# Kernel optimization log

Hardware: AMD Instinct MI355X
Metric: run time of the kernel (lower is better)

The kernel has to match this reference:

```python
import jax, jax.numpy as jnp
import numpy as np

B, M, NT, V, D, H, E, S = 4, 12, 12, 10000, 64, 3, 512, 32


def setup_inputs() -> dict:
    key = jax.random.key(0)
    ks = jax.random.split(key, 16)
    def rn(k, shape, scale=0.05):
        return jax.random.normal(k, shape, dtype=jnp.float32) * scale
    return {
        "tendency": jax.random.normal(ks[0], (B, M, V), dtype=jnp.float32),
        "periodicity": jax.random.normal(ks[1], (B, NT, V), dtype=jnp.float32),
        "edges": jax.random.randint(ks[2], (H, E, S), 0, V),
        "w1": rn(ks[3], (1, D)), "b1": rn(ks[4], (D,)),
        "w2": rn(ks[5], (D, D)), "b2": rn(ks[6], (D,)),
        "attn_w": rn(ks[7], (D, D)), "attn_a": rn(ks[8], (2 * D, 1)),
        "w_ih": rn(ks[9], (4 * D, D)), "w_hh": rn(ks[10], (4 * D, D)),
        "b_ih": rn(ks[11], (4 * D,)), "b_hh": rn(ks[12], (4 * D,)),
        "w_out": rn(ks[13], (2 * D, 1)), "b_out": rn(ks[14], (1,)),
    }


def _hypersage(X, edges, w, b):
    # X: (N, V, F); edges: (E, S) node indices. All edges have size S <= Q,
    # so torch's random subsampling is the identity.
    n, v, f = X.shape
    e, s = edges.shape
    gathered = X[:, edges, :]                      # (N, E, S, F)
    agg = gathered.mean(axis=2)                    # (N, E, F)
    flat = edges.reshape(-1)                       # (E*S,)
    contrib = jnp.broadcast_to(agg[:, :, None, :], (n, e, s, f)).reshape(n, e * s, f)
    X_out = jnp.zeros((n, v, f), X.dtype).at[:, flat, :].add(contrib)
    deg = jnp.zeros((v,), X.dtype).at[flat].add(1.0)
    deg = jnp.maximum(deg, 1.0)
    X_out = X_out / deg[None, :, None]
    return X_out @ w + b                           # Linear fc


def _attention(Xs, attn_w, attn_a):
    # Xs: (H, N, V, D)
    ref = Xs.mean(axis=0)                          # (N, V, D)
    wx = Xs @ attn_w                               # (H, N, V, D)
    wr = ref @ attn_w                              # (N, V, D)
    z = jnp.concatenate([wx, jnp.broadcast_to(wr[None], wx.shape)], axis=-1) @ attn_a
    z = jax.nn.leaky_relu(z, negative_slope=0.2)   # (H, N, V, 1)
    alpha = jax.nn.softmax(z, axis=0)
    return (alpha * Xs).sum(axis=0)                # (N, V, D)


def _lstm_final(x, w_ih, w_hh, b_ih, b_hh):
    # x: (BV, T, D) -> final hidden state (BV, D). PyTorch gate order i,f,g,o.
    bv, t, d = x.shape
    xg = x @ w_ih.T + (b_ih + b_hh)                # precompute input gates (BV, T, 4D)
    def step(carry, xg_t):
        h, c = carry
        g = xg_t + h @ w_hh.T
        i, f, gg, o = jnp.split(g, 4, axis=-1)
        c = jax.nn.sigmoid(f) * c + jax.nn.sigmoid(i) * jnp.tanh(gg)
        h = jax.nn.sigmoid(o) * jnp.tanh(c)
        return (h, c), None
    h0 = jnp.zeros((bv, d), x.dtype)
    (h, _), _ = jax.lax.scan(step, (h0, h0), jnp.swapaxes(xg, 0, 1))
    return h


def _branch(seq, edges, w1, b1, w2, b2, attn_w, attn_a, w_ih, w_hh, b_ih, b_hh):
    b, t, v = seq.shape
    X = seq.reshape(b * t, v, 1)                   # fold time into batch (same DAMHG per step)
    def per_hg(e):
        return _hypersage(_hypersage(X, e, w1, b1), e, w2, b2)
    xs = jax.vmap(per_hg)(edges)                   # (H, B*T, V, D)
    fused = _attention(xs, attn_w, attn_a)         # (B*T, V, D)
    d = fused.shape[-1]
    seq_v = fused.reshape(b, t, v, d).transpose(0, 2, 1, 3).reshape(b * v, t, d)
    h = _lstm_final(seq_v, w_ih, w_hh, b_ih, b_hh)
    return h.reshape(b, v, d)


def reference(tendency, periodicity, edges, w1, b1, w2, b2, attn_w, attn_a, w_ih, w_hh, b_ih, b_hh, w_out, b_out):
    h_t = _branch(tendency, edges, w1, b1, w2, b2, attn_w, attn_a, w_ih, w_hh, b_ih, b_hh)
    h_p = _branch(periodicity, edges, w1, b1, w2, b2, attn_w, attn_a, w_ih, w_hh, b_ih, b_hh)
    fusion = jnp.concatenate([h_t, h_p], axis=-1)  # (B, V, 2D)
    out = fusion @ w_out + b_out                   # (B, V, 1)
    return out[..., 0]
```

## Files before the change

### kernel.cpp

```cpp
#include <hip/hip_runtime.h>

#define NV 10000
#define NB 4
#define NTT 12
#define NSEQ 48
#define NH 3
#define NE 512
#define NS 32
#define ND 64

#define S_U   0
#define S_C1  64
#define S_V1  128
#define S_V2  192
#define S_SC  256
#define S_GU  272
#define S_GC  528
#define S_G0  784
#define F_INV 1040
#define F_M   (F_INV + NH*NV)
#define F_PQ  (F_M + NH*NV)
#define F_HT  (F_PQ + 4*NV*NSEQ)
#define I_CNT (F_HT + 2*NB*NV)
#define I_CUR (I_CNT + NH*NV)
#define I_OFF (I_CUR + NH*NV)
#define I_SLOT (I_OFF + NH*NV)
#define F_DYN (I_SLOT + NH*NE*NS)
#define XT_SZ  (NV*NSEQ)
#define AGG_SZ (NH*NE*NSEQ)
#define YZ_SZ  (NH*NV*NSEQ)

typedef __attribute__((ext_vector_type(8))) _Float16 f16x8;
typedef __attribute__((ext_vector_type(4))) float f32x4;

__device__ __forceinline__ float sigf(float x) {
  return __builtin_amdgcn_rcpf(1.0f + __expf(-x));
}
__device__ __forceinline__ float tanh_fast(float x) {
  return 1.0f - 2.0f * __builtin_amdgcn_rcpf(1.0f + __expf(2.0f * x));
}
__device__ __forceinline__ unsigned short f2h(float x) {
  union { _Float16 h; unsigned short u; } c;
  c.h = (_Float16)x;
  return c.u;
}
__device__ __forceinline__ f16x8 ldsH(const unsigned short* p) {
  union { uint4 u; f16x8 v; } x;
  x.u = *(const uint4*)p;
  return x.v;
}

__global__ void k_prep(const float* __restrict__ w1, const float* __restrict__ b1,
                       const float* __restrict__ w2, const float* __restrict__ b2,
                       const float* __restrict__ attn_w, const float* __restrict__ attn_a,
                       const float* __restrict__ w_ih, const float* __restrict__ b_ih,
                       const float* __restrict__ b_hh, float* __restrict__ ws) {
  __shared__ float u_s[64], c1_s[64];
  const int tid = threadIdx.x;
  if (tid < 64) {
    float v1 = 0.f, v2 = 0.f, u = 0.f, c1 = 0.f;
    for (int d = 0; d < 64; ++d) {
      const float aw = attn_w[tid * 64 + d];
      v1 += aw * attn_a[d];
      v2 += aw * attn_a[64 + d];
      const float w2v = w2[d * 64 + tid];
      u  += w1[d] * w2v;
      c1 += b1[d] * w2v;
    }
    ws[S_U + tid] = u;  ws[S_C1 + tid] = c1;
    ws[S_V1 + tid] = v1; ws[S_V2 + tid] = v2;
    u_s[tid] = u; c1_s[tid] = c1;
  }
  __syncthreads();
  if (tid == 0) {
    float al = 0.f, be = 0.f, ga = 0.f, de = 0.f, ep = 0.f;
    for (int d = 0; d < 64; ++d) {
      const float v1 = ws[S_V1 + d], v2 = ws[S_V2 + d];
      al += u_s[d] * v1;  be += c1_s[d] * v1;
      ga += u_s[d] * v2;  de += c1_s[d] * v2;
      ep += b2[d] * (v1 + v2);
    }
    ws[S_SC + 0] = al; ws[S_SC + 1] = be; ws[S_SC + 2] = ga;
    ws[S_SC + 3] = de; ws[S_SC + 4] = ep;
  }
  {
    const int j = tid;
    float gu = 0.f, gc = 0.f, g0 = 0.f;
    for (int d = 0; d < 64; ++d) {
      const float w = w_ih[j * 64 + d];
      gu += w * u_s[d]; gc += w * c1_s[d]; g0 += w * b2[d];
    }
    ws[S_GU + j] = gu; ws[S_GC + j] = gc;
    ws[S_G0 + j] = g0 + b_ih[j] + b_hh[j];
  }
}

__global__ void k_zero(int* __restrict__ p, int n) {
  const int g = blockIdx.x * 256 + threadIdx.x;
  if (g < n) p[g] = 0;
}

__global__ void k_count(const int* __restrict__ edges, int* __restrict__ counts) {
  const int g = blockIdx.x * 256 + threadIdx.x;
  if (g >= NH * NE * NS) return;
  const int h = g >> 14;
  atomicAdd(&counts[h * NV + edges[g]], 1);
}

__global__ void k_scan(const int* __restrict__ counts, int* __restrict__ offs,
                       float* __restrict__ invdeg, float* __restrict__ mvec) {
  const int h = blockIdx.x;
  const int tid = threadIdx.x;
  const int base = h * NV;
  const int CH = 10;
  int local[10];
  int run = 0;
  for (int i = 0; i < CH; ++i) {
    const int v = tid * CH + i;
    const int c = (v < NV) ? counts[base + v] : 0;
    local[i] = run; run += c;
  }
  __shared__ int sd[1024];
  sd[tid] = run;
  __syncthreads();
  int acc = run;
  for (int off = 1; off < 1024; off <<= 1) {
    const int t = (tid >= off) ? sd[tid - off] : 0;
    __syncthreads();
    acc += t; sd[tid] = acc;
    __syncthreads();
  }
  const int excl = acc - run;
  for (int i = 0; i < CH; ++i) {
    const int v = tid * CH + i;
    if (v < NV) {
      offs[base + v] = excl + local[i];
      const int c = counts[base + v];
      invdeg[base + v] = 1.0f / (float)((c > 0) ? c : 1);
      mvec[base + v] = (c > 0) ? 1.0f : 0.0f;
    }
  }
}

__global__ void k_fill(const int* __restrict__ edges, const int* __restrict__ offs,
                       int* __restrict__ cursor, int* __restrict__ slot_edge) {
  const int g = blockIdx.x * 256 + threadIdx.x;
  if (g >= NH * NE * NS) return;
  const int h = g >> 14;
  const int e = (g >> 5) & (NE - 1);
  const int v = edges[g];
  const int pos = atomicAdd(&cursor[h * NV + v], 1);
  slot_edge[h * NE * NS + offs[h * NV + v] + pos] = e;
}

__global__ void k_trans2(const float* __restrict__ s0, const float* __restrict__ s1,
                         float* __restrict__ xT, int xtS) {
  __shared__ float tile[128][49];
  const float* seq = blockIdx.y ? s1 : s0;
  float* o = xT + (size_t)blockIdx.y * xtS;
  const int v0 = blockIdx.x * 128;
  const int tid = threadIdx.x;
  for (int i = tid; i < 128 * NSEQ; i += 256) {
    const int n = i / 128, vl = i % 128;
    const int v = v0 + vl;
    tile[vl][n] = (v < NV) ? seq[n * NV + v] : 0.0f;
  }
  __syncthreads();
  for (int i = tid; i < 128 * NSEQ; i += 256) {
    const int vl = i / NSEQ, n = i % NSEQ;
    const int v = v0 + vl;
    if (v < NV) o[v * NSEQ + n] = tile[vl][n];
  }
}

__global__ void k_eagg1(const int* __restrict__ edges, const float* __restrict__ xT,
                        int xtS, float* __restrict__ agg, int aggS) {
  const int g = blockIdx.x * 256 + threadIdx.x;
  if (g >= NH * NE * 12) return;
  const float* x = xT + (size_t)blockIdx.y * xtS;
  float* a = agg + (size_t)blockIdx.y * aggS;
  const int n0 = (g % 12) * 4;
  const int e = (g / 12) % NE;
  const int h = g / (12 * NE);
  const int* ep = edges + (h * NE + e) * NS;
  float4 acc = make_float4(0.f, 0.f, 0.f, 0.f);
  for (int s = 0; s < NS; ++s) {
    const float4 t = *(const float4*)&x[ep[s] * NSEQ + n0];
    acc.x += t.x; acc.y += t.y; acc.z += t.z; acc.w += t.w;
  }
  acc.x *= (1.0f / NS); acc.y *= (1.0f / NS); acc.z *= (1.0f / NS); acc.w *= (1.0f / NS);
  *(float4*)&a[(h * NE + e) * NSEQ + n0] = acc;
}

__global__ void k_eagg2(const int* __restrict__ edges, const float* __restrict__ ysum,
                        int yS, const float* __restrict__ invdeg,
                        float* __restrict__ agg, int aggS) {
  const int g = blockIdx.x * 256 + threadIdx.x;
  if (g >= NH * NE * 12) return;
  const float* y = ysum + (size_t)blockIdx.y * yS;
  float* a = agg + (size_t)blockIdx.y * aggS;
  const int n0 = (g % 12) * 4;
  const int e = (g / 12) % NE;
  const int h = g / (12 * NE);
  const int* ep = edges + (h * NE + e) * NS;
  float4 acc = make_float4(0.f, 0.f, 0.f, 0.f);
  for (int s = 0; s < NS; ++s) {
    const int v = ep[s];
    const float iv = invdeg[h * NV + v];
    const float4 t = *(const float4*)&y[(h * NV + v) * NSEQ + n0];
    acc.x += t.x * iv; acc.y += t.y * iv; acc.z += t.z * iv; acc.w += t.w * iv;
  }
  acc.x *= (1.0f / NS); acc.y *= (1.0f / NS); acc.z *= (1.0f / NS); acc.w *= (1.0f / NS);
  *(float4*)&a[(h * NE + e) * NSEQ + n0] = acc;
}

__global__ void k_vg(const int* __restrict__ counts, const int* __restrict__ offs,
                     const int* __restrict__ slot_edge, const float* __restrict__ agg,
                     int aggS, float* __restrict__ outv, int outS) {
  const int g = blockIdx.x * 256 + threadIdx.x;
  if (g >= NH * NV * 12) return;
  const float* a = agg + (size_t)blockIdx.y * aggS;
  float* o = outv + (size_t)blockIdx.y * outS;
  const int n0 = (g % 12) * 4;
  const int v = (g / 12) % NV;
  const int h = g / (12 * NV);
  const int beg = offs[h * NV + v];
  const int cnt = counts[h * NV + v];
  const int* se = slot_edge + h * NE * NS;
  float4 acc = make_float4(0.f, 0.f, 0.f, 0.f);
  for (int i = 0; i < cnt; ++i) {
    const int e = se[beg + i];
    const float4 t = *(const float4*)&a[(h * NE + e) * NSEQ + n0];
    acc.x += t.x; acc.y += t.y; acc.z += t.z; acc.w += t.w;
  }
  *(float4*)&o[(h * NV + v) * NSEQ + n0] = acc;
}

__global__ void k_attn(const float* __restrict__ zsum, int zS,
                       const float* __restrict__ invdeg, const float* __restrict__ mvec,
                       const float* __restrict__ ws, float* __restrict__ pq, int br0) {
  const int g = blockIdx.x * 256 + threadIdx.x;
  if (g >= NV * 12) return;
  const int bi = blockIdx.y;
  const float* z = zsum + (size_t)bi * zS;
  float* pbuf = pq + (size_t)(bi + br0) * 2 * NV * NSEQ;
  float* qbuf = pbuf + NV * NSEQ;
  const int n0 = (g % 12) * 4;
  const int v = g / 12;
  const float al = ws[S_SC + 0], be = ws[S_SC + 1], ga = ws[S_SC + 2],
              de = ws[S_SC + 3], ep = ws[S_SC + 4];
  union { float4 v4; float f[4]; } zh[3], pv, qv;
  float mh[3];
  #pragma unroll
  for (int h = 0; h < NH; ++h) {
    const float iv = invdeg[h * NV + v];
    float4 t = *(const float4*)&z[(h * NV + v) * NSEQ + n0];
    t.x *= iv; t.y *= iv; t.z *= iv; t.w *= iv;
    zh[h].v4 = t;
    mh[h] = mvec[h * NV + v];
  }
  const float mb = (mh[0] + mh[1] + mh[2]) * (1.f / 3.f);
  #pragma unroll
  for (int j = 0; j < 4; ++j) {
    const float z0 = zh[0].f[j], z1 = zh[1].f[j], z2 = zh[2].f[j];
    const float zb = (z0 + z1 + z2) * (1.f / 3.f);
    float sc[3];
    const float zt[3] = {z0, z1, z2};
    #pragma unroll
    for (int h = 0; h < NH; ++h) {
      const float s = al * zt[h] + be * mh[h] + ga * zb + de * mb + ep;
      sc[h] = (s > 0.f) ? s : 0.2f * s;
    }
    const float mx = fmaxf(sc[0], fmaxf(sc[1], sc[2]));
    const float e0 = __expf(sc[0] - mx), e1 = __expf(sc[1] - mx), e2 = __expf(sc[2] - mx);
    const float inv = 1.0f / (e0 + e1 + e2);
    pv.f[j] = (e0 * z0 + e1 * z1 + e2 * z2) * inv;
    qv.f[j] = (e0 * mh[0] + e1 * mh[1] + e2 * mh[2]) * inv;
  }
  *(float4*)&pbuf[v * NSEQ + n0] = pv.v4;
  *(float4*)&qbuf[v * NSEQ + n0] = qv.v4;
}

#define RS2 72
__launch_bounds__(256, 2)
__global__ void k_lstm2(const float* __restrict__ w_hh, const float* __restrict__ ws,
                        const float* __restrict__ pbase, const float* __restrict__ w_out,
                        float* __restrict__ part) {
  __shared__ __align__(16) unsigned short smem[16384];
  __shared__ float ps_sh[NTT][64], qs_sh[NTT][64];
  const int tid = threadIdx.x;
  const int w = tid >> 6, lane = tid & 63, q = lane >> 4, l15 = lane & 15;
  const int b = blockIdx.y, br = blockIdx.z;
  const int v0 = blockIdx.x * 64;
  const int d = w * 16 + l15;

  for (int i = tid; i < 4096; i += 256) {
    const float4 w4 = ((const float4*)w_hh)[i];
    const int j = i >> 4, k = (i & 15) * 4;
    uint2 pk;
    pk.x = (unsigned int)f2h(w4.x) | ((unsigned int)f2h(w4.y) << 16);
    pk.y = (unsigned int)f2h(w4.z) | ((unsigned int)f2h(w4.w) << 16);
    *(uint2*)&smem[j * 64 + k] = pk;
  }
  const float* pp = pbase + (size_t)br * 2 * NV * NSEQ;
  const float* qq = pp + NV * NSEQ;
  for (int i = tid; i < 384; i += 256) {
    const int arr = (i >= 192) ? 1 : 0;
    const int ii = i - arr * 192;
    const int s = ii / 3, f4 = ii % 3;
    const int v = v0 + s;
    const float* src = arr ? qq : pp;
    float4 val = make_float4(0.f, 0.f, 0.f, 0.f);
    if (v < NV) val = *(const float4*)&src[v * NSEQ + b * NTT + f4 * 4];
    float (*dst)[64] = arr ? qs_sh : ps_sh;
    dst[f4 * 4 + 0][s] = val.x; dst[f4 * 4 + 1][s] = val.y;
    dst[f4 * 4 + 2][s] = val.z; dst[f4 * 4 + 3][s] = val.w;
  }
  __syncthreads();

  f16x8 Bf[4][2];
  #pragma unroll
  for (int g = 0; g < 4; ++g)
    #pragma unroll
    for (int kh = 0; kh < 2; ++kh)
      Bf[g][kh] = ldsH(&smem[(g * 64 + d) * 64 + kh * 32 + q * 8]);

  union HU { uint4 u; f16x8 v; };
  HU bex[4];
  #pragma unroll
  for (int g = 0; g < 4; ++g) {
    const float gu = ws[S_GU + g * 64 + d];
    const float gc = ws[S_GC + g * 64 + d];
    const float g0 = ws[S_G0 + g * 64 + d];
    bex[g].u.x = (q == 0) ? ((unsigned int)f2h(gu) | ((unsigned int)f2h(gc) << 16)) : 0u;
    bex[g].u.y = (q == 0) ? (unsigned int)f2h(g0) : 0u;
    bex[g].u.z = 0u; bex[g].u.w = 0u;
  }
  const float WO = w_out[br * 64 + d];
  __syncthreads();

  f32x4 acc[4][4];
  f32x4 cst[4];
  float pr[4][4];
  #pragma unroll
  for (int mi = 0; mi < 4; ++mi) cst[mi] = (f32x4){0.f, 0.f, 0.f, 0.f};
  const f32x4 z4 = (f32x4){0.f, 0.f, 0.f, 0.f};

  #pragma unroll 1
  for (int t = 0; t < NTT; ++t) {
    #pragma unroll
    for (int mi = 0; mi < 4; ++mi) {
      HU ae;
      const float pv = ps_sh[t][mi * 16 + l15];
      const float qv = qs_sh[t][mi * 16 + l15];
      ae.u.x = (q == 0) ? ((unsigned int)f2h(pv) | ((unsigned int)f2h(qv) << 16)) : 0u;
      ae.u.y = (q == 0) ? 0x3C00u : 0u;
      ae.u.z = 0u; ae.u.w = 0u;
      #pragma unroll
      for (int g = 0; g < 4; ++g)
        acc[mi][g] = __builtin_amdgcn_mfma_f32_16x16x32_f16(ae.v, bex[g].v, z4, 0, 0, 0);
    }
    if (t > 0) {
      const unsigned short* hr = smem + ((t - 1) & 1) * (64 * RS2);
      #pragma unroll
      for (int kh = 0; kh < 2; ++kh)
        #pragma unroll
        for (int mi = 0; mi < 4; ++mi) {
          const int row = mi * 16 + l15;
          const f16x8 Ah = ldsH(&hr[row * RS2 + kh * 32 + q * 8]);
          #pragma unroll
          for (int g = 0; g < 4; ++g)
            acc[mi][g] = __builtin_amdgcn_mfma_f32_16x16x32_f16(Ah, Bf[g][kh], acc[mi][g], 0, 0, 0);
        }
    }
    unsigned short* hw = smem + (t & 1) * (64 * RS2);
    const bool last = (t == NTT - 1);
    #pragma unroll
    for (int mi = 0; mi < 4; ++mi)
      #pragma unroll
      for (int r = 0; r < 4; ++r) {
        const float ig = sigf(acc[mi][0][r]);
        const float fg = sigf(acc[mi][1][r]);
        const float gg = tanh_fast(acc[mi][2][r]);
        const float og = sigf(acc[mi][3][r]);
        const float cn = fmaf(fg, cst[mi][r], ig * gg);
        cst[mi][r] = cn;
        const float h = og * tanh_fast(cn);
        const int s = mi * 16 + q * 4 + r;
        if (!last) {
          hw[s * RS2 + d] = f2h(h);
        } else {
          pr[mi][r] = h * WO;
        }
      }
    __syncthreads();
  }
  float* fbuf = (float*)smem;
  #pragma unroll
  for (int mi = 0; mi < 4; ++mi)
    #pragma unroll
    for (int r = 0; r < 4; ++r) {
      float v = pr[mi][r];
      v += __shfl_xor(v, 1);
      v += __shfl_xor(v, 2);
      v += __shfl_xor(v, 4);
      v += __shfl_xor(v, 8);
      if (l15 == 0) fbuf[w * 64 + mi * 16 + q * 4 + r] = v;
    }
  __syncthreads();
  if (tid < 64) {
    const int v = v0 + tid;
    if (v < NV)
      part[(br * NB + b) * NV + v] =
          fbuf[tid] + fbuf[64 + tid] + fbuf[128 + tid] + fbuf[192 + tid];
  }
}

__global__ void k_comb(const float* __restrict__ part, const float* __restrict__ b_out,
                       float* __restrict__ out) {
  const int g = blockIdx.x * 256 + threadIdx.x;
  if (g >= NB * NV / 4) return;
  const float4 a = ((const float4*)part)[g];
  const float4 c = ((const float4*)part)[NB * NV / 4 + g];
  const float bo = b_out[0];
  float4 o;
  o.x = a.x + c.x + bo; o.y = a.y + c.y + bo;
  o.z = a.z + c.z + bo; o.w = a.w + c.w + bo;
  ((float4*)out)[g] = o;
}

extern "C" void kernel_launch(void* const* d_in, const int* in_sizes, int n_in,
                              void* d_out, int out_size, void* d_ws, size_t ws_size,
                              hipStream_t stream) {
  const float* tend   = (const float*)d_in[0];
  const float* peri   = (const float*)d_in[1];
  const int*   edges  = (const int*)d_in[2];
  const float* w1     = (const float*)d_in[3];
  const float* b1     = (const float*)d_in[4];
  const float* w2     = (const float*)d_in[5];
  const float* b2     = (const float*)d_in[6];
  const float* attn_w = (const float*)d_in[7];
  const float* attn_a = (const float*)d_in[8];
  const float* w_ih   = (const float*)d_in[9];
  const float* w_hh   = (const float*)d_in[10];
  const float* b_ih   = (const float*)d_in[11];
  const float* b_hh   = (const float*)d_in[12];
  const float* w_out  = (const float*)d_in[13];
  const float* b_out  = (const float*)d_in[14];
  float* out = (float*)d_out;
  float* ws  = (float*)d_ws;
  int*   iws = (int*)d_ws;
  int* cnt = iws + I_CNT;
  int* cur = iws + I_CUR;
  int* off = iws + I_OFF;
  int* sed = iws + I_SLOT;

  const size_t need2 = ((size_t)F_DYN + 2 * (XT_SZ + AGG_SZ + YZ_SZ)) * 4;
  const bool batched = ws_size >= need2;
  const int nb = batched ? 2 : 1;
  float* XT  = ws + F_DYN;
  float* AGG = XT + (size_t)nb * XT_SZ;
  float* YZ  = AGG + (size_t)nb * AGG_SZ;

  k_prep<<<1, 256, 0, stream>>>(w1, b1, w2, b2, attn_w, attn_a, w_ih, b_ih, b_hh, ws);
  k_zero<<<(2 * NH * NV + 255) / 256, 256, 0, stream>>>(cnt, 2 * NH * NV);
  k_count<<<(NH * NE * NS) / 256, 256, 0, stream>>>(edges, cnt);
  k_scan<<<NH, 1024, 0, stream>>>(cnt, off, ws + F_INV, ws + F_M);
  k_fill<<<(NH * NE * NS) / 256, 256, 0, stream>>>(edges, off, cur, sed);

  const int g_eagg = (NH * NE * 12 + 255) / 256;
  const int g_vg   = (NH * NV * 12 + 255) / 256;
  const int g_attn = (NV * 12 + 255) / 256;
  if (batched) {
    k_trans2<<<dim3((NV + 127) / 128, 2), 256, 0, stream>>>(tend, peri, XT, XT_SZ);
    k_eagg1<<<dim3(g_eagg, 2), 256, 0, stream>>>(edges, XT, XT_SZ, AGG, AGG_SZ);
    k_vg<<<dim3(g_vg, 2), 256, 0, stream>>>(cnt, off, sed, AGG, AGG_SZ, YZ, YZ_SZ);
    k_eagg2<<<dim3(g_eagg, 2), 256, 0, stream>>>(edges, YZ, YZ_SZ, ws + F_INV, AGG, AGG_SZ);
    k_vg<<<dim3(g_vg, 2), 256, 0, stream>>>(cnt, off, sed, AGG, AGG_SZ, YZ, YZ_SZ);
    k_attn<<<dim3(g_attn, 2), 256, 0, stream>>>(YZ, YZ_SZ, ws + F_INV, ws + F_M, ws, ws + F_PQ, 0);
  } else {
    for (int br = 0; br < 2; ++br) {
      const float* seq = br ? peri : tend;
      k_trans2<<<dim3((NV + 127) / 128, 1), 256, 0, stream>>>(seq, seq, XT, 0);
      k_eagg1<<<dim3(g_eagg, 1), 256, 0, stream>>>(edges, XT, 0, AGG, 0);
      k_vg<<<dim3(g_vg, 1), 256, 0, stream>>>(cnt, off, sed, AGG, 0, YZ, 0);
      k_eagg2<<<dim3(g_eagg, 1), 256, 0, stream>>>(edges, YZ, 0, ws + F_INV, AGG, 0);
      k_vg<<<dim3(g_vg, 1), 256, 0, stream>>>(cnt, off, sed, AGG, 0, YZ, 0);
      k_attn<<<dim3(g_attn, 1), 256, 0, stream>>>(YZ, 0, ws + F_INV, ws + F_M, ws, ws + F_PQ, br);
    }
  }
  dim3 lgrid((NV + 63) / 64, NB, 2);
  k_lstm2<<<lgrid, 256, 0, stream>>>(w_hh, ws, ws + F_PQ, w_out, ws + F_HT);
  k_comb<<<(NB * NV / 4 + 255) / 256, 256, 0, stream>>>(ws + F_HT, b_out, out);
}
```

Before: 262.0 us.

## Shrink LSTM LDS, load recurrent weights directly, interleave gates per row block

```diff
diff --git a/kernel.cpp b/kernel.cpp
--- a/kernel.cpp
+++ b/kernel.cpp
@@ -36,9 +36,6 @@
 __device__ __forceinline__ float sigf(float x) {
   return __builtin_amdgcn_rcpf(1.0f + __expf(-x));
 }
-__device__ __forceinline__ float tanh_fast(float x) {
-  return 1.0f - 2.0f * __builtin_amdgcn_rcpf(1.0f + __expf(2.0f * x));
-}
 __device__ __forceinline__ unsigned short f2h(float x) {
   union { _Float16 h; unsigned short u; } c;
   c.h = (_Float16)x;
@@ -282,11 +279,11 @@
 }
 
 #define RS2 72
-__launch_bounds__(256, 2)
+__launch_bounds__(256, 4)
 __global__ void k_lstm2(const float* __restrict__ w_hh, const float* __restrict__ ws,
                         const float* __restrict__ pbase, const float* __restrict__ w_out,
                         float* __restrict__ part) {
-  __shared__ __align__(16) unsigned short smem[16384];
+  __shared__ __align__(16) unsigned short smem[2 * 64 * RS2];
   __shared__ float ps_sh[NTT][64], qs_sh[NTT][64];
   const int tid = threadIdx.x;
   const int w = tid >> 6, lane = tid & 63, q = lane >> 4, l15 = lane & 15;
@@ -294,14 +291,8 @@
   const int v0 = blockIdx.x * 64;
   const int d = w * 16 + l15;
 
-  for (int i = tid; i < 4096; i += 256) {
-    const float4 w4 = ((const float4*)w_hh)[i];
-    const int j = i >> 4, k = (i & 15) * 4;
-    uint2 pk;
-    pk.x = (unsigned int)f2h(w4.x) | ((unsigned int)f2h(w4.y) << 16);
-    pk.y = (unsigned int)f2h(w4.z) | ((unsigned int)f2h(w4.w) << 16);
-    *(uint2*)&smem[j * 64 + k] = pk;
-  }
+  union HU { uint4 u; f16x8 v; };
+
   const float* pp = pbase + (size_t)br * 2 * NV * NSEQ;
   const float* qq = pp + NV * NSEQ;
   for (int i = tid; i < 384; i += 256) {
@@ -316,16 +307,23 @@
     dst[f4 * 4 + 0][s] = val.x; dst[f4 * 4 + 1][s] = val.y;
     dst[f4 * 4 + 2][s] = val.z; dst[f4 * 4 + 3][s] = val.w;
   }
-  __syncthreads();
 
   f16x8 Bf[4][2];
   #pragma unroll
   for (int g = 0; g < 4; ++g)
     #pragma unroll
-    for (int kh = 0; kh < 2; ++kh)
-      Bf[g][kh] = ldsH(&smem[(g * 64 + d) * 64 + kh * 32 + q * 8]);
-
-  union HU { uint4 u; f16x8 v; };
+    for (int kh = 0; kh < 2; ++kh) {
+      const float* wp = w_hh + (g * 64 + d) * 64 + kh * 32 + q * 8;
+      const float4 lo = *(const float4*)wp;
+      const float4 hi = *(const float4*)(wp + 4);
+      HU f;
+      f.u.x = (unsigned int)f2h(lo.x) | ((unsigned int)f2h(lo.y) << 16);
+      f.u.y = (unsigned int)f2h(lo.z) | ((unsigned int)f2h(lo.w) << 16);
+      f.u.z = (unsigned int)f2h(hi.x) | ((unsigned int)f2h(hi.y) << 16);
+      f.u.w = (unsigned int)f2h(hi.z) | ((unsigned int)f2h(hi.w) << 16);
+      Bf[g][kh] = f.v;
+    }
+
   HU bex[4];
   #pragma unroll
   for (int g = 0; g < 4; ++g) {
@@ -339,7 +337,6 @@
   const float WO = w_out[br * 64 + d];
   __syncthreads();
 
-  f32x4 acc[4][4];
   f32x4 cst[4];
   float pr[4][4];
   #pragma unroll
@@ -348,6 +345,9 @@
 
   #pragma unroll 1
   for (int t = 0; t < NTT; ++t) {
+    const unsigned short* hr = smem + ((t + 1) & 1) * (64 * RS2);
+    unsigned short* hw = smem + (t & 1) * (64 * RS2);
+    const bool last = (t == NTT - 1);
     #pragma unroll
     for (int mi = 0; mi < 4; ++mi) {
       HU ae;
@@ -356,43 +356,40 @@
       ae.u.x = (q == 0) ? ((unsigned int)f2h(pv) | ((unsigned int)f2h(qv) << 16)) : 0u;
       ae.u.y = (q == 0) ? 0x3C00u : 0u;
       ae.u.z = 0u; ae.u.w = 0u;
-      #pragma unroll
-      for (int g = 0; g < 4; ++g)
-        acc[mi][g] = __builtin_amdgcn_mfma_f32_16x16x32_f16(ae.v, bex[g].v, z4, 0, 0, 0);
-    }
-    if (t > 0) {
-      const unsigned short* hr = smem + ((t - 1) & 1) * (64 * RS2);
-      #pragma unroll
-      for (int kh = 0; kh < 2; ++kh)
+      f32x4 aI = __builtin_amdgcn_mfma_f32_16x16x32_f16(ae.v, bex[0].v, z4, 0, 0, 0);
+      f32x4 aF = __builtin_amdgcn_mfma_f32_16x16x32_f16(ae.v, bex[1].v, z4, 0, 0, 0);
+      f32x4 aG = __builtin_amdgcn_mfma_f32_16x16x32_f16(ae.v, bex[2].v, z4, 0, 0, 0);
+      f32x4 aO = __builtin_amdgcn_mfma_f32_16x16x32_f16(ae.v, bex[3].v, z4, 0, 0, 0);
+      if (t > 0) {
         #pragma unroll
-        for (int mi = 0; mi < 4; ++mi) {
-          const int row = mi * 16 + l15;
-          const f16x8 Ah = ldsH(&hr[row * RS2 + kh * 32 + q * 8]);
-          #pragma unroll
-          for (int g = 0; g < 4; ++g)
-            acc[mi][g] = __builtin_amdgcn_mfma_f32_16x16x32_f16(Ah, Bf[g][kh], acc[mi][g], 0, 0, 0);
+        for (int kh = 0; kh < 2; ++kh) {
+          const f16x8 Ah = ldsH(&hr[(mi * 16 + l15) * RS2 + kh * 32 + q * 8]);
+          aI = __builtin_amdgcn_mfma_f32_16x16x32_f16(Ah, Bf[0][kh], aI, 0, 0, 0);
+          aF = __builtin_amdgcn_mfma_f32_16x16x32_f16(Ah, Bf[1][kh], aF, 0, 0, 0);
+          aG = __builtin_amdgcn_mfma_f32_16x16x32_f16(Ah, Bf[2][kh], aG, 0, 0, 0);
+          aO = __builtin_amdgcn_mfma_f32_16x16x32_f16(Ah, Bf[3][kh], aO, 0, 0, 0);
         }
-    }
-    unsigned short* hw = smem + (t & 1) * (64 * RS2);
-    const bool last = (t == NTT - 1);
-    #pragma unroll
-    for (int mi = 0; mi < 4; ++mi)
+      }
       #pragma unroll
       for (int r = 0; r < 4; ++r) {
-        const float ig = sigf(acc[mi][0][r]);
-        const float fg = sigf(acc[mi][1][r]);
-        const float gg = tanh_fast(acc[mi][2][r]);
-        const float og = sigf(acc[mi][3][r]);
-        const float cn = fmaf(fg, cst[mi][r], ig * gg);
+        const float ea = __expf(-aI[r]);
+        const float eb = __expf(-2.0f * aG[r]);
+        const float igg = (1.0f - eb) *
+            __builtin_amdgcn_rcpf((1.0f + ea) * (1.0f + eb));
+        const float fg = sigf(aF[r]);
+        const float cn = fmaf(fg, cst[mi][r], igg);
         cst[mi][r] = cn;
-        const float h = og * tanh_fast(cn);
-        const int s = mi * 16 + q * 4 + r;
+        const float ec = __expf(-aO[r]);
+        const float ed = __expf(-2.0f * cn);
+        const float h = (1.0f - ed) *
+            __builtin_amdgcn_rcpf((1.0f + ec) * (1.0f + ed));
         if (!last) {
-          hw[s * RS2 + d] = f2h(h);
+          hw[(mi * 16 + q * 4 + r) * RS2 + d] = f2h(h);
         } else {
           pr[mi][r] = h * WO;
         }
       }
+    }
     __syncthreads();
   }
   float* fbuf = (float*)smem;
```

Result: no change. 256.9 us (-1.9%).
